# Optimization experiments

Hardware: AMD Instinct MI355X
Metric: run time of the kernel (lower is better)

## Reference

```python
import jax, jax.numpy as jnp
import numpy as np
import math

NUM_HEADS = 12
BLOCK_N = 32  # key-block size used by the Triton kernel for head_dim <= 64


def _apply_rope(x, cos, sin):
    # x: [B,H,S,D]; cos/sin: [S, D//2] -> interleaved-pair RoPE (matches apply_rope_rse)
    c = cos[None, None, :, :]
    s = sin[None, None, :, :]
    xe = x[..., 0::2]
    xo = x[..., 1::2]
    re = xe * c - xo * s
    ro = xo * c + xe * s
    return jnp.stack([re, ro], axis=-1).reshape(x.shape)


def setup_inputs() -> dict:
    key = jax.random.key(0)
    ks = jax.random.split(key, 9)
    B, S, HID = 16, 1024, 768
    D = HID // NUM_HEADS
    x = jax.random.normal(ks[0], (B, S, HID), jnp.float32)
    init = lambda k: jax.random.normal(k, (HID, HID), jnp.float32) * 0.02
    Wq, Wk, Wv, Wo = init(ks[1]), init(ks[2]), init(ks[3]), init(ks[4])
    bq = jnp.zeros((HID,), jnp.float32)
    bk = jnp.zeros((HID,), jnp.float32)
    bv = jnp.zeros((HID,), jnp.float32)
    bo = jnp.zeros((HID,), jnp.float32)
    lam = jnp.array(0.01, jnp.float32)
    # RoPE caches [S, D//2]
    inv_freq = 1.0 / (10000.0 ** (jnp.arange(0, D, 2, dtype=jnp.float32) / D))
    ang = jnp.arange(S, dtype=jnp.float32)[:, None] * inv_freq[None, :]
    cos_cache = jnp.cos(ang)
    sin_cache = jnp.sin(ang)
    return {"x": x, "Wq": Wq, "bq": bq, "Wk": Wk, "bk": bk, "Wv": Wv, "bv": bv,
            "Wo": Wo, "bo": bo, "lam": lam, "cos_cache": cos_cache, "sin_cache": sin_cache}


def _rse_attention(q, k, v, cos_cache, sin_cache, lam):
    # q,k,v: [B,H,S,D]. Block-sequential stick-breaking with online stats,
    # faithfully reproducing the Triton kernel's math (causal=False).
    B, H, S, D = q.shape
    scale = 1.0 / math.sqrt(D)
    qs = _apply_rope(q, cos_cache, sin_cache) * scale
    kr = _apply_rope(k, cos_cache, sin_cache)
    nb = S // BLOCK_N
    kb = jnp.moveaxis(kr.reshape(B, H, nb, BLOCK_N, D), 2, 0)  # [nb,B,H,BN,D]
    vb = jnp.moveaxis(v.reshape(B, H, nb, BLOCK_N, D), 2, 0)   # [nb,B,H,BN,D]
    pos_m = jnp.arange(S, dtype=jnp.float32)
    pb = jnp.arange(S, dtype=jnp.float32).reshape(nb, BLOCK_N)

    def step(carry, inp):
        rem, acc, l_i, m_i = carry
        kblk, vblk, pblk = inp
        decay = lam * jnp.abs(pos_m[:, None] - pblk[None, :])  # [S,BN]
        logits = jnp.einsum('bhmd,bhnd->bhmn', qs, kblk) - decay[None, None]
        beta = jax.nn.sigmoid(jnp.clip(logits, -20.0, 20.0))
        w = beta * rem[..., None]                 # [B,H,S,BN]
        consumed = jnp.sum(w, axis=-1)            # [B,H,S]
        rem_new = jnp.maximum(rem * (1.0 - consumed), 1e-6)
        acc_new = acc + jnp.einsum('bhmn,bhnd->bhmd', w, vblk)
        m_new = jnp.maximum(m_i, jnp.max(logits, axis=-1))
        alpha = jnp.exp2(m_i - m_new)
        l_new = l_i * alpha + consumed
        return (rem_new, acc_new, l_new, m_new), None

    rem0 = jnp.ones((B, H, S), jnp.float32)
    acc0 = jnp.zeros((B, H, S, D), jnp.float32)
    l0 = jnp.zeros((B, H, S), jnp.float32)
    m0 = jnp.full((B, H, S), -jnp.inf, jnp.float32)
    (rem, acc, l_i, m_i), _ = jax.lax.scan(step, (rem0, acc0, l0, m0), (kb, vb, pb))
    return acc / jnp.maximum(l_i, 1e-6)[..., None]


def reference(x, Wq, bq, Wk, bk, Wv, bv, Wo, bo, lam, cos_cache, sin_cache):
    B, S, HID = x.shape
    H = NUM_HEADS
    D = HID // H
    to_heads = lambda t: t.reshape(B, S, H, D).transpose(0, 2, 1, 3)
    q = to_heads(x @ Wq.T + bq)
    k = to_heads(x @ Wk.T + bk)
    v = to_heads(x @ Wv.T + bv)
    o = _rse_attention(q, k, v, cos_cache, sin_cache, lam)  # [B,H,S,D]
    ctx = o.transpose(0, 2, 1, 3).reshape(B, S, HID)
    return ctx @ Wo.T + bo
```

## Files before the change

kernel.cpp:

```cpp
#include <hip/hip_runtime.h>
#include <math.h>

#define NH    12
#define SEQ   1024
#define DH    64
#define HID   768
#define BATCH 16
#define MTOT  (BATCH*SEQ)
#define KDIM  HID

typedef __attribute__((ext_vector_type(8))) short short8;
typedef __attribute__((ext_vector_type(4))) short short4v;
typedef __attribute__((ext_vector_type(8))) unsigned short ushort8;
typedef __attribute__((ext_vector_type(4))) float float4v;

__device__ __forceinline__ float bf2f(unsigned short u) {
    union { unsigned int i; float f; } v; v.i = ((unsigned int)u) << 16; return v.f;
}
__device__ __forceinline__ unsigned short f2bf(float f) {
    union { float f; unsigned int i; } v; v.f = f;
    unsigned int x = v.i;
    return (unsigned short)((x + 0x7FFFu + ((x >> 16) & 1u)) >> 16);
}
__device__ __forceinline__ float loadf(const void* p, size_t i, bool f32) {
    return f32 ? ((const float*)p)[i] : bf2f(((const unsigned short*)p)[i]);
}
__device__ __forceinline__ unsigned int cvt_pk_bf16(float a, float b) {
    unsigned int r;
    asm("v_cvt_pk_bf16_f32 %0, %1, %2" : "=v"(r) : "v"(a), "v"(b));
    return r;
}
__device__ __forceinline__ float fast_exp2(float x) {
#if __has_builtin(__builtin_amdgcn_exp2f)
    return __builtin_amdgcn_exp2f(x);
#else
    return exp2f(x);
#endif
}

__device__ __forceinline__ void gload_lds16(const void* g, void* l) {
    __builtin_amdgcn_global_load_lds(
        (const __attribute__((address_space(1))) unsigned int*)g,
        (__attribute__((address_space(3))) unsigned int*)l, 16, 0, 0);
}

__global__ __launch_bounds__(256) void detect_kernel(
    const unsigned short* __restrict__ x, unsigned int* __restrict__ flag)
{
    __shared__ int cnt[256];
    const int tid = threadIdx.x;
    int local = 0;
    for (int i = tid; i < 1024; i += 256) {
        const unsigned short u = x[i];
        const int e = (u >> 7) & 0xFF;
        if ((e >= 96 && e <= 134) || ((u & 0x7FFF) == 0)) local++;
    }
    cnt[tid] = local;
    __syncthreads();
    for (int s = 128; s > 0; s >>= 1) {
        if (tid < s) cnt[tid] += cnt[tid + s];
        __syncthreads();
    }
    if (tid == 0) flag[0] = (cnt[0] < 900) ? 1u : 0u;
}

template<bool LO>
__global__ __launch_bounds__(256) void split_ker(
    const void* __restrict__ src, const unsigned int* __restrict__ flag,
    unsigned short* __restrict__ hi, unsigned short* __restrict__ lo, int n)
{
    const size_t i = ((size_t)blockIdx.x * 256 + threadIdx.x) * 8;
    if (i >= (size_t)n) return;
    ushort8 h, l;
    if (flag[0]) {
        const float* fp = (const float*)src + i;
        float4v f0 = *(const float4v*)fp, f1 = *(const float4v*)(fp + 4);
#pragma unroll
        for (int e = 0; e < 4; e++) {
            unsigned short h0 = f2bf(f0[e]), h1 = f2bf(f1[e]);
            h[e] = h0; h[4 + e] = h1;
            if (LO) { l[e] = f2bf(f0[e] - bf2f(h0)); l[4 + e] = f2bf(f1[e] - bf2f(h1)); }
        }
    } else {
        h = *(const ushort8*)((const unsigned short*)src + i);
        if (LO) {
#pragma unroll
            for (int e = 0; e < 8; e++) l[e] = 0;
        }
    }
    *(ushort8*)(hi + i) = h;
    if (LO) *(ushort8*)(lo + i) = l;
}

template<bool WF32, bool PRECISE>
__device__ __forceinline__ void loadW(const void* __restrict__ W, size_t idx,
                                      short8& hi, short8& lo) {
    if constexpr (WF32) {
        const float* fp = (const float*)W + idx;
        float4v f0 = *(const float4v*)fp, f1 = *(const float4v*)(fp + 4);
#pragma unroll
        for (int e = 0; e < 4; e++) {
            unsigned short h0 = f2bf(f0[e]), h1 = f2bf(f1[e]);
            hi[e] = (short)h0; hi[4 + e] = (short)h1;
            if constexpr (PRECISE) {
                lo[e] = (short)f2bf(f0[e] - bf2f(h0));
                lo[4 + e] = (short)f2bf(f1[e] - bf2f(h1));
            }
        }
    } else {
        hi = *(const short8*)((const unsigned short*)W + idx);
        if constexpr (PRECISE) {
#pragma unroll
            for (int e = 0; e < 8; e++) lo[e] = 0;
        }
    }
}

template<bool PRECISE, bool WPRE, bool WF32>
__device__ __forceinline__ void staged_kloop(
    const unsigned short* __restrict__ Ahi, const unsigned short* __restrict__ Alo,
    const void* __restrict__ Wa, const void* __restrict__ Wb,
    unsigned short* sAhi, unsigned short* sAlo,
    int m_blk0, int n_base, int wid, int lane, float4v acc[4][4])
{
    const int tid  = wid * 64 + lane;
    const int quad = lane >> 4, l16 = lane & 15;
    const int m_off = (wid >> 1) * 64;
    const int srow = tid >> 2;
    const int scc  = tid & 3;

    auto stage = [&](int k0, int b) {
#pragma unroll
        for (int it = 0; it < 2; it++) {
            const int r = it * 64 + srow;
            const size_t gidx = (size_t)(m_blk0 + r) * KDIM + k0 + scc * 8;
            const int loff = b * 4096 + r * 32 + scc * 8;
            gload_lds16(Ahi + gidx, sAhi + loff);
            if constexpr (PRECISE) gload_lds16(Alo + gidx, sAlo + loff);
        }
    };

    stage(0, 0);
    __syncthreads();

    for (int k0 = 0; k0 < KDIM; k0 += 32) {
        const int b = (k0 >> 5) & 1;
        if (k0 + 32 < KDIM) stage(k0 + 32, b ^ 1);

        short8 bh[4], bl[4];
#pragma unroll
        for (int in = 0; in < 4; in++) {
            const size_t widx = (size_t)(n_base + in * 16 + l16) * KDIM + k0 + quad * 8;
            if constexpr (WPRE) {
                bh[in] = *(const short8*)((const unsigned short*)Wa + widx);
                if constexpr (PRECISE)
                    bl[in] = *(const short8*)((const unsigned short*)Wb + widx);
            } else {
                loadW<WF32, PRECISE>(Wa, widx, bh[in], bl[in]);
            }
        }
        short8 ah[4], al[4];
#pragma unroll
        for (int im = 0; im < 4; im++) {
            const int r = m_off + im * 16 + l16;
            ah[im] = *(const short8*)(sAhi + b * 4096 + r * 32 + quad * 8);
            if constexpr (PRECISE) al[im] = *(const short8*)(sAlo + b * 4096 + r * 32 + quad * 8);
        }
#pragma unroll
        for (int im = 0; im < 4; im++)
#pragma unroll
            for (int in = 0; in < 4; in++) {
                acc[im][in] = __builtin_amdgcn_mfma_f32_16x16x32_bf16(
                    ah[im], bh[in], acc[im][in], 0, 0, 0);
                if constexpr (PRECISE) {
                    acc[im][in] = __builtin_amdgcn_mfma_f32_16x16x32_bf16(
                        al[im], bh[in], acc[im][in], 0, 0, 0);
                    acc[im][in] = __builtin_amdgcn_mfma_f32_16x16x32_bf16(
                        ah[im], bl[in], acc[im][in], 0, 0, 0);
                }
            }
        __syncthreads();
    }
}

template<int MODE, bool WPRE>
__device__ __forceinline__ void gemm_body(
    const unsigned short* __restrict__ Ahi, const unsigned short* __restrict__ Alo,
    const void* __restrict__ Wa, const void* __restrict__ Wb,
    const void* __restrict__ bias,
    const void* __restrict__ cosc, const void* __restrict__ sinc,
    const unsigned int* __restrict__ flag,
    void* __restrict__ Out, void* __restrict__ Out2,
    unsigned short* sAhi, unsigned short* sAlo,
    int m_blk0, int ny)
{
    constexpr bool PRECISE = (MODE <= 1);
    const int tid  = threadIdx.x;
    const int wid  = tid >> 6;
    const int lane = tid & 63;
    const int quad = lane >> 4;
    const int l16  = lane & 15;
    const int m_blk = m_blk0 + (wid >> 1) * 64;
    const int n_base = ny * 128 + (wid & 1) * 64;
    const bool f32 = (flag[0] != 0u);

    float4v acc[4][4];
#pragma unroll
    for (int i = 0; i < 4; i++)
#pragma unroll
        for (int j = 0; j < 4; j++) acc[i][j] = (float4v)(0.f);

    if constexpr (WPRE) {
        staged_kloop<PRECISE, true, false>(Ahi, Alo, Wa, Wb, sAhi, sAlo,
                                           m_blk0, n_base, wid, lane, acc);
    } else {
        if (f32) staged_kloop<PRECISE, false, true >(Ahi, Alo, Wa, Wb, sAhi, sAlo,
                                                     m_blk0, n_base, wid, lane, acc);
        else     staged_kloop<PRECISE, false, false>(Ahi, Alo, Wa, Wb, sAhi, sAlo,
                                                     m_blk0, n_base, wid, lane, acc);
    }

#pragma unroll
    for (int im = 0; im < 4; im++) {
#pragma unroll
        for (int in = 0; in < 4; in++) {
            const int col = n_base + in * 16 + l16;
            const float bval = loadf(bias, col, f32);
            if constexpr (MODE == 2) {
                short4v pk;
#pragma unroll
                for (int r = 0; r < 4; r++)
                    pk[r] = (short)f2bf(acc[im][in][r] + bval);
                const int row = m_blk + im * 16 + quad * 4;
                const int b = row >> 10, s = row & (SEQ - 1);
                const int h = col >> 6, d = col & (DH - 1);
                *(short4v*)((unsigned short*)Out +
                    ((size_t)(b * NH + h) * DH + d) * SEQ + s) = pk;
            } else if constexpr (MODE <= 1) {
                const int d  = col & (DH - 1);
                const int d2 = d >> 1;
#pragma unroll
                for (int r = 0; r < 4; r++) {
                    const int row = m_blk + im * 16 + quad * 4 + r;
                    const int s  = row & (SEQ - 1);
                    const float v = acc[im][in][r] + bval;
                    const float c  = loadf(cosc, s * (DH / 2) + d2, f32);
                    const float sn = loadf(sinc, s * (DH / 2) + d2, f32);
                    const float p = __shfl_xor(v, 1);
                    float o = (d & 1) ? (v * c + p * sn) : (v * c - p * sn);
                    if (MODE == 0) o *= 0.18033688f;
                    const float po = __shfl_xor(o, 1);
                    if (!(l16 & 1)) {
                        const unsigned short h0 = f2bf(o), h1 = f2bf(po);
                        const unsigned short l0 = f2bf(o - bf2f(h0));
                        const unsigned short l1 = f2bf(po - bf2f(h1));
                        const int b = row >> 10, h = col >> 6;
                        const size_t idx = ((size_t)(b * NH + h) * SEQ + s) * DH + d;
                        *(unsigned int*)((unsigned short*)Out + idx) =
                            (unsigned int)h0 | ((unsigned int)h1 << 16);
                        *(unsigned int*)((unsigned short*)Out2 + idx) =
                            (unsigned int)l0 | ((unsigned int)l1 << 16);
                    }
                }
            } else {
#pragma unroll
                for (int r = 0; r < 4; r++) {
                    const int row = m_blk + im * 16 + quad * 4 + r;
                    const float v = acc[im][in][r] + bval;
                    if (f32) ((float*)Out)[(size_t)row * HID + col] = v;
                    else     ((unsigned short*)Out)[(size_t)row * HID + col] = f2bf(v);
                }
            }
        }
    }
}

template<int MODE, bool WPRE>
__global__ __launch_bounds__(256) void gemm_staged(
    const unsigned short* __restrict__ Ahi, const unsigned short* __restrict__ Alo,
    const void* __restrict__ Wa, const void* __restrict__ Wb,
    const void* __restrict__ bias,
    const void* __restrict__ cosc, const void* __restrict__ sinc,
    const unsigned int* __restrict__ flag,
    void* __restrict__ Out, void* __restrict__ Out2)
{
    constexpr bool PRECISE = (MODE <= 1);
    __shared__ unsigned short sAhi[2 * 4096];
    __shared__ unsigned short sAlo[PRECISE ? 2 * 4096 : 64];
    gemm_body<MODE, WPRE>(Ahi, Alo, Wa, Wb, bias, cosc, sinc, flag, Out, Out2,
                          sAhi, sAlo, blockIdx.x * 128, blockIdx.y);
}

template<bool WPRE>
__global__ __launch_bounds__(256) void gemm_qkv(
    const unsigned short* __restrict__ Ahi, const unsigned short* __restrict__ Alo,
    const void* __restrict__ Wqa, const void* __restrict__ Wqb,
    const void* __restrict__ Wka, const void* __restrict__ Wkb,
    const void* __restrict__ Wva,
    const void* __restrict__ bq, const void* __restrict__ bk,
    const void* __restrict__ bv,
    const void* __restrict__ cosc, const void* __restrict__ sinc,
    const unsigned int* __restrict__ flag,
    void* __restrict__ Qhi, void* __restrict__ Qlo,
    void* __restrict__ Khi, void* __restrict__ Klo,
    void* __restrict__ Vt)
{
    __shared__ unsigned short sAhi[2 * 4096];
    __shared__ unsigned short sAlo[2 * 4096];
    const int which = blockIdx.y / 6;
    const int ny    = blockIdx.y % 6;
    const int m0    = blockIdx.x * 128;
    if (which == 0)
        gemm_body<0, WPRE>(Ahi, Alo, Wqa, Wqb, bq, cosc, sinc, flag,
                           Qhi, Qlo, sAhi, sAlo, m0, ny);
    else if (which == 1)
        gemm_body<1, WPRE>(Ahi, Alo, Wka, Wkb, bk, cosc, sinc, flag,
                           Khi, Klo, sAhi, sAlo, m0, ny);
    else
        gemm_body<2, WPRE>(Ahi, nullptr, Wva, nullptr, bv, nullptr, nullptr, flag,
                           Vt, nullptr, sAhi, sAlo, m0, ny);
}

__global__ __launch_bounds__(256, 2) void attn_mfma(
    const unsigned short* __restrict__ Qhi, const unsigned short* __restrict__ Qlo,
    const unsigned short* __restrict__ Khi, const unsigned short* __restrict__ Klo,
    const unsigned short* __restrict__ Vt,
    const void* __restrict__ lam_p, const unsigned int* __restrict__ flag,
    unsigned short* __restrict__ ctx)
{
    const int tid  = threadIdx.x;
    const int wid  = tid >> 6;
    const int lane = tid & 63;
    const int quad = lane >> 4;
    const int l16  = lane & 15;
    const int phys = blockIdx.x;
    const int virt = (phys & 7) * 96 + (phys >> 3);
    const int bh   = virt >> 2;
    const int q0   = (virt & 3) * 256 + wid * 64;
    const bool f32 = (flag[0] != 0u);
    const float lam2 = loadf(lam_p, 0, f32) * 1.44269504f;

    __shared__ unsigned short KV[2][6144];

    const int krow = tid >> 3, kch = tid & 7;
    const int kgch = kch ^ (krow & 7);
    const int vrow = tid >> 2, vch = tid & 3;
    const int vgch = vch ^ (vrow & 3);

    #define STAGE(kb_, buf_) do {                                            \
        const size_t gk = ((size_t)bh * SEQ + (kb_) * 32 + krow) * DH + kgch * 8; \
        gload_lds16(Khi + gk, &KV[buf_][0]    + tid * 8);                    \
        gload_lds16(Klo + gk, &KV[buf_][2048] + tid * 8);                    \
        const size_t gv = ((size_t)bh * DH + vrow) * SEQ + (kb_) * 32 + vgch * 8; \
        gload_lds16(Vt + gv, &KV[buf_][4096] + tid * 8);                     \
    } while (0)

    short8 qh[4][2], ql[4][2];
#pragma unroll
    for (int qn = 0; qn < 4; qn++)
#pragma unroll
        for (int ks = 0; ks < 2; ks++) {
            const size_t base = ((size_t)bh * SEQ + (q0 + qn * 16 + l16)) * DH
                                + ks * 32 + quad * 8;
            qh[qn][ks] = *(const short8*)(Qhi + base);
            ql[qn][ks] = *(const short8*)(Qlo + base);
        }

    float4v acc_o[4][4];
#pragma unroll
    for (int i = 0; i < 4; i++)
#pragma unroll
        for (int j = 0; j < 4; j++) acc_o[i][j] = (float4v)(0.f);

    float rem[4] = {1.f, 1.f, 1.f, 1.f};
    float l_i[4] = {0.f, 0.f, 0.f, 0.f};
    float m_i[4] = {-INFINITY, -INFINITY, -INFINITY, -INFINITY};
    float qf[4];
#pragma unroll
    for (int qn = 0; qn < 4; qn++) qf[qn] = (float)(q0 + qn * 16 + l16);

    STAGE(0, 0);
    __syncthreads();

    for (int kb = 0; kb < SEQ / 32; kb++) {
        const int buf = kb & 1;
        if (kb + 1 < SEQ / 32) STAGE(kb + 1, buf ^ 1);

        short8 kh[2][2], kl[2][2];
#pragma unroll
        for (int kt = 0; kt < 2; kt++)
#pragma unroll
            for (int ks = 0; ks < 2; ks++) {
                const int off = (kt * 16 + l16) * 64
                                + ((ks * 4 + quad) ^ (l16 & 7)) * 8;
                kh[kt][ks] = *(const short8*)(&KV[buf][0]    + off);
                kl[kt][ks] = *(const short8*)(&KV[buf][2048] + off);
            }

        float4v s[2][4];
#pragma unroll
        for (int kt = 0; kt < 2; kt++)
#pragma unroll
            for (int qn = 0; qn < 4; qn++) s[kt][qn] = (float4v)(0.f);
#pragma unroll
        for (int ks = 0; ks < 2; ks++)
#pragma unroll
            for (int kt = 0; kt < 2; kt++)
#pragma unroll
                for (int qn = 0; qn < 4; qn++) {
                    s[kt][qn] = __builtin_amdgcn_mfma_f32_16x16x32_bf16(
                        kh[kt][ks], qh[qn][ks], s[kt][qn], 0, 0, 0);
                    s[kt][qn] = __builtin_amdgcn_mfma_f32_16x16x32_bf16(
                        kl[kt][ks], qh[qn][ks], s[kt][qn], 0, 0, 0);
                    s[kt][qn] = __builtin_amdgcn_mfma_f32_16x16x32_bf16(
                        kh[kt][ks], ql[qn][ks], s[kt][qn], 0, 0, 0);
                }

        float cons[4] = {0.f, 0.f, 0.f, 0.f};
        float mx[4] = {-INFINITY, -INFINITY, -INFINITY, -INFINITY};
#pragma unroll
        for (int kt = 0; kt < 2; kt++)
#pragma unroll
            for (int qn = 0; qn < 4; qn++)
#pragma unroll
                for (int r = 0; r < 4; r++) {
                    const float keyf = (float)(kb * 32 + kt * 16 + quad * 4 + r);
                    const float logit = s[kt][qn][r] - lam2 * fabsf(qf[qn] - keyf);
                    mx[qn] = fmaxf(mx[qn], logit);
                    const float beta = __builtin_amdgcn_rcpf(
                        1.f + fast_exp2(-logit));
                    const float w = beta * rem[qn];
                    cons[qn] += w;
                    s[kt][qn][r] = w;
                }
#pragma unroll
        for (int qn = 0; qn < 4; qn++) {
            cons[qn] += __shfl_xor(cons[qn], 16);
            cons[qn] += __shfl_xor(cons[qn], 32);
            mx[qn] = fmaxf(mx[qn], __shfl_xor(mx[qn], 16));
            mx[qn] = fmaxf(mx[qn], __shfl_xor(mx[qn], 32));
        }

        short8 pf[4];
#pragma unroll
        for (int qn = 0; qn < 4; qn++) {
            const unsigned int d00 = cvt_pk_bf16(s[0][qn][0], s[0][qn][1]);
            const unsigned int d01 = cvt_pk_bf16(s[0][qn][2], s[0][qn][3]);
            const unsigned int d10 = cvt_pk_bf16(s[1][qn][0], s[1][qn][1]);
            const unsigned int d11 = cvt_pk_bf16(s[1][qn][2], s[1][qn][3]);
            auto r0 = __builtin_amdgcn_permlane32_swap(d00, d10, false, false);
            auto r1 = __builtin_amdgcn_permlane32_swap(d01, d11, false, false);
            auto t0 = __builtin_amdgcn_permlane16_swap(r0[0], r0[1], false, false);
            auto t1 = __builtin_amdgcn_permlane16_swap(r1[0], r1[1], false, false);
            union { unsigned int u[4]; short8 s8; } cv;
            cv.u[0] = t0[0];
            cv.u[1] = t1[0];
            cv.u[2] = t0[1];
            cv.u[3] = t1[1];
            pf[qn] = cv.s8;
        }

        short8 vf[4];
#pragma unroll
        for (int dt = 0; dt < 4; dt++) {
            const int off = (dt * 16 + l16) * 32 + (quad ^ (l16 & 3)) * 8;
            vf[dt] = *(const short8*)(&KV[buf][4096] + off);
        }
#pragma unroll
        for (int dt = 0; dt < 4; dt++)
#pragma unroll
            for (int jn = 0; jn < 4; jn++)
                acc_o[dt][jn] = __builtin_amdgcn_mfma_f32_16x16x32_bf16(
                    vf[dt], pf[jn], acc_o[dt][jn], 0, 0, 0);

#pragma unroll
        for (int qn = 0; qn < 4; qn++) {
            rem[qn] = fmaxf(rem[qn] * (1.f - cons[qn]), 1e-6f);
            const float m_new = fmaxf(m_i[qn], mx[qn]);
            const float alpha = fast_exp2((m_i[qn] - m_new) * 0.69314718f);
            l_i[qn] = l_i[qn] * alpha + cons[qn];
            m_i[qn] = m_new;
        }

        __syncthreads();
    }

    const int b = bh / NH, h = bh % NH;
    float inv[4];
#pragma unroll
    for (int jn = 0; jn < 4; jn++)
        inv[jn] = __builtin_amdgcn_rcpf(fmaxf(l_i[jn], 1e-6f));
#pragma unroll
    for (int dt = 0; dt < 4; dt++)
#pragma unroll
        for (int jn = 0; jn < 4; jn++) {
            short4v pk;
#pragma unroll
            for (int r = 0; r < 4; r++)
                pk[r] = (short)f2bf(acc_o[dt][jn][r] * inv[jn]);
            const int q_g = q0 + jn * 16 + l16;
            *(short4v*)(ctx + ((size_t)(b * SEQ + q_g) * HID
                               + h * DH + dt * 16 + quad * 4)) = pk;
        }
    #undef STAGE
}

extern "C" void kernel_launch(void* const* d_in, const int* in_sizes, int n_in,
                              void* d_out, int out_size, void* d_ws, size_t ws_size,
                              hipStream_t stream) {
    const void* x    = d_in[0];
    const void* Wq   = d_in[1];
    const void* bq   = d_in[2];
    const void* Wk   = d_in[3];
    const void* bk   = d_in[4];
    const void* Wv   = d_in[5];
    const void* bv   = d_in[6];
    const void* Wo   = d_in[7];
    const void* bo   = d_in[8];
    const void* lam  = d_in[9];
    const void* cosc = d_in[10];
    const void* sinc = d_in[11];

    const size_t NELEM = (size_t)MTOT * HID;
    const size_t WELEM = (size_t)HID * HID;
    unsigned int* flag = (unsigned int*)d_ws;
    unsigned short* Xhi = (unsigned short*)((char*)d_ws + 64);
    unsigned short* Xlo = Xhi + NELEM;
    unsigned short* Qhi = Xlo + NELEM;
    unsigned short* Qlo = Qhi + NELEM;
    unsigned short* Wqh = Qlo + NELEM;
    unsigned short* Wql = Wqh + WELEM;
    unsigned short* Wkh = Wql + WELEM;
    unsigned short* Wkl = Wkh + WELEM;
    unsigned short* Wvh = Wkl + WELEM;
    unsigned short* Woh = Wvh + WELEM;
    unsigned short* VtF = Woh + WELEM;
    const size_t NEED  = 64 + 4 * NELEM * 2 + 6 * WELEM * 2;
    const size_t NEEDF = NEED + NELEM * 2;
    const bool wpre = (ws_size >= NEED);
    const bool fuse = (ws_size >= NEEDF);

    unsigned short* Vt  = fuse ? VtF : Xlo;
    unsigned short* Ctx = Xhi;
    unsigned short* Khi = (unsigned short*)d_out;
    unsigned short* Klo = Khi + NELEM;

    detect_kernel<<<1, 256, 0, stream>>>((const unsigned short*)x, flag);
    split_ker<true><<<(MTOT * KDIM) / 2048, 256, 0, stream>>>(x, flag, Xhi, Xlo, MTOT * KDIM);

    dim3 gg(MTOT / 128, HID / 128), gb(256);
    if (fuse) {
        const int wb = (int)(WELEM / 2048);
        split_ker<true ><<<wb, 256, 0, stream>>>(Wq, flag, Wqh, Wql, (int)WELEM);
        split_ker<true ><<<wb, 256, 0, stream>>>(Wk, flag, Wkh, Wkl, (int)WELEM);
        split_ker<false><<<wb, 256, 0, stream>>>(Wv, flag, Wvh, nullptr, (int)WELEM);
        split_ker<false><<<wb, 256, 0, stream>>>(Wo, flag, Woh, nullptr, (int)WELEM);
        gemm_qkv<true><<<dim3(MTOT / 128, 18), gb, 0, stream>>>(
            Xhi, Xlo, Wqh, Wql, Wkh, Wkl, Wvh, bq, bk, bv,
            cosc, sinc, flag, Qhi, Qlo, Khi, Klo, VtF);
    } else if (wpre) {
        const int wb = (int)(WELEM / 2048);
        split_ker<true ><<<wb, 256, 0, stream>>>(Wq, flag, Wqh, Wql, (int)WELEM);
        split_ker<true ><<<wb, 256, 0, stream>>>(Wk, flag, Wkh, Wkl, (int)WELEM);
        split_ker<false><<<wb, 256, 0, stream>>>(Wv, flag, Wvh, nullptr, (int)WELEM);
        split_ker<false><<<wb, 256, 0, stream>>>(Wo, flag, Woh, nullptr, (int)WELEM);
        gemm_staged<0, true><<<gg, gb, 0, stream>>>(Xhi, Xlo, Wqh, Wql, bq, cosc, sinc, flag, Qhi, Qlo);
        gemm_staged<1, true><<<gg, gb, 0, stream>>>(Xhi, Xlo, Wkh, Wkl, bk, cosc, sinc, flag, Khi, Klo);
        gemm_staged<2, true><<<gg, gb, 0, stream>>>(Xhi, nullptr, Wvh, nullptr, bv, nullptr, nullptr, flag, Vt, nullptr);
    } else {
        gemm_staged<0, false><<<gg, gb, 0, stream>>>(Xhi, Xlo, Wq, nullptr, bq, cosc, sinc, flag, Qhi, Qlo);
        gemm_staged<1, false><<<gg, gb, 0, stream>>>(Xhi, Xlo, Wk, nullptr, bk, cosc, sinc, flag, Khi, Klo);
        gemm_staged<2, false><<<gg, gb, 0, stream>>>(Xhi, nullptr, Wv, nullptr, bv, nullptr, nullptr, flag, Vt, nullptr);
    }
    attn_mfma<<<dim3(4 * BATCH * NH), 256, 0, stream>>>(
        Qhi, Qlo, Khi, Klo, Vt, lam, flag, Ctx);
    if (wpre)
        gemm_staged<3, true><<<gg, gb, 0, stream>>>(Ctx, nullptr, Woh, nullptr, bo, nullptr, nullptr, flag, d_out, nullptr);
    else
        gemm_staged<3, false><<<gg, gb, 0, stream>>>(Ctx, nullptr, Wo, nullptr, bo, nullptr, nullptr, flag, d_out, nullptr);
}
```

Before: 665.9 us.

## Load GEMM A operands directly from global and interleave independent MFMA chains

Replaces the LDS double-buffered staging of the A operand in the projection GEMMs with direct per-wave global loads of the MFMA fragments. This removes the shared memory allocation and the per-iteration block barrier. In exchange, reuse of A across the two column-half waves now comes from cache instead of LDS. It also reorders the MFMA sequences in both the GEMM and the attention score computation, so that consecutive instructions target different accumulators rather than chaining on the same one, which is meant to hide MFMA dependency latency.

```diff
diff --git a/kernel.cpp b/kernel.cpp
--- a/kernel.cpp
+++ b/kernel.cpp
@@ -117,40 +117,32 @@
 }
 
 template<bool PRECISE, bool WPRE, bool WF32>
-__device__ __forceinline__ void staged_kloop(
+__device__ __forceinline__ void direct_kloop(
     const unsigned short* __restrict__ Ahi, const unsigned short* __restrict__ Alo,
     const void* __restrict__ Wa, const void* __restrict__ Wb,
-    unsigned short* sAhi, unsigned short* sAlo,
-    int m_blk0, int n_base, int wid, int lane, float4v acc[4][4])
-{
-    const int tid  = wid * 64 + lane;
+    int m_blk, int n_base, int lane, float4v acc[4][4])
+{
     const int quad = lane >> 4, l16 = lane & 15;
-    const int m_off = (wid >> 1) * 64;
-    const int srow = tid >> 2;
-    const int scc  = tid & 3;
-
-    auto stage = [&](int k0, int b) {
-#pragma unroll
-        for (int it = 0; it < 2; it++) {
-            const int r = it * 64 + srow;
-            const size_t gidx = (size_t)(m_blk0 + r) * KDIM + k0 + scc * 8;
-            const int loff = b * 4096 + r * 32 + scc * 8;
-            gload_lds16(Ahi + gidx, sAhi + loff);
-            if constexpr (PRECISE) gload_lds16(Alo + gidx, sAlo + loff);
-        }
-    };
-
-    stage(0, 0);
-    __syncthreads();
-
-    for (int k0 = 0; k0 < KDIM; k0 += 32) {
-        const int b = (k0 >> 5) & 1;
-        if (k0 + 32 < KDIM) stage(k0 + 32, b ^ 1);
-
+    constexpr int NT = KDIM / 32;
+
+    const unsigned short* A0h = Ahi + (size_t)(m_blk + l16) * KDIM;
+    const unsigned short* A0l = Alo ? Alo + (size_t)(m_blk + l16) * KDIM : nullptr;
+
+#pragma unroll 2
+    for (int kt = 0; kt < NT; kt++) {
+        const int kc = kt * 32 + quad * 8;
+
+        short8 ah[4], al[4];
+#pragma unroll
+        for (int im = 0; im < 4; im++) {
+            ah[im] = *(const short8*)(A0h + (size_t)(im * 16) * KDIM + kc);
+            if constexpr (PRECISE)
+                al[im] = *(const short8*)(A0l + (size_t)(im * 16) * KDIM + kc);
+        }
         short8 bh[4], bl[4];
 #pragma unroll
         for (int in = 0; in < 4; in++) {
-            const size_t widx = (size_t)(n_base + in * 16 + l16) * KDIM + k0 + quad * 8;
+            const size_t widx = (size_t)(n_base + in * 16 + l16) * KDIM + kc;
             if constexpr (WPRE) {
                 bh[in] = *(const short8*)((const unsigned short*)Wa + widx);
                 if constexpr (PRECISE)
@@ -159,27 +151,26 @@
                 loadW<WF32, PRECISE>(Wa, widx, bh[in], bl[in]);
             }
         }
-        short8 ah[4], al[4];
-#pragma unroll
-        for (int im = 0; im < 4; im++) {
-            const int r = m_off + im * 16 + l16;
-            ah[im] = *(const short8*)(sAhi + b * 4096 + r * 32 + quad * 8);
-            if constexpr (PRECISE) al[im] = *(const short8*)(sAlo + b * 4096 + r * 32 + quad * 8);
-        }
 #pragma unroll
         for (int im = 0; im < 4; im++)
 #pragma unroll
-            for (int in = 0; in < 4; in++) {
+            for (int in = 0; in < 4; in++)
                 acc[im][in] = __builtin_amdgcn_mfma_f32_16x16x32_bf16(
                     ah[im], bh[in], acc[im][in], 0, 0, 0);
-                if constexpr (PRECISE) {
+        if constexpr (PRECISE) {
+#pragma unroll
+            for (int im = 0; im < 4; im++)
+#pragma unroll
+                for (int in = 0; in < 4; in++)
                     acc[im][in] = __builtin_amdgcn_mfma_f32_16x16x32_bf16(
                         al[im], bh[in], acc[im][in], 0, 0, 0);
+#pragma unroll
+            for (int im = 0; im < 4; im++)
+#pragma unroll
+                for (int in = 0; in < 4; in++)
                     acc[im][in] = __builtin_amdgcn_mfma_f32_16x16x32_bf16(
                         ah[im], bl[in], acc[im][in], 0, 0, 0);
-                }
-            }
-        __syncthreads();
+        }
     }
 }
 
@@ -191,7 +182,6 @@
     const void* __restrict__ cosc, const void* __restrict__ sinc,
     const unsigned int* __restrict__ flag,
     void* __restrict__ Out, void* __restrict__ Out2,
-    unsigned short* sAhi, unsigned short* sAlo,
     int m_blk0, int ny)
 {
     constexpr bool PRECISE = (MODE <= 1);
@@ -211,13 +201,13 @@
         for (int j = 0; j < 4; j++) acc[i][j] = (float4v)(0.f);
 
     if constexpr (WPRE) {
-        staged_kloop<PRECISE, true, false>(Ahi, Alo, Wa, Wb, sAhi, sAlo,
-                                           m_blk0, n_base, wid, lane, acc);
+        direct_kloop<PRECISE, true, false>(Ahi, Alo, Wa, Wb,
+                                           m_blk, n_base, lane, acc);
     } else {
-        if (f32) staged_kloop<PRECISE, false, true >(Ahi, Alo, Wa, Wb, sAhi, sAlo,
-                                                     m_blk0, n_base, wid, lane, acc);
-        else     staged_kloop<PRECISE, false, false>(Ahi, Alo, Wa, Wb, sAhi, sAlo,
-                                                     m_blk0, n_base, wid, lane, acc);
+        if (f32) direct_kloop<PRECISE, false, true >(Ahi, Alo, Wa, Wb,
+                                                     m_blk, n_base, lane, acc);
+        else     direct_kloop<PRECISE, false, false>(Ahi, Alo, Wa, Wb,
+                                                     m_blk, n_base, lane, acc);
     }
 
 #pragma unroll
@@ -284,11 +274,8 @@
     const unsigned int* __restrict__ flag,
     void* __restrict__ Out, void* __restrict__ Out2)
 {
-    constexpr bool PRECISE = (MODE <= 1);
-    __shared__ unsigned short sAhi[2 * 4096];
-    __shared__ unsigned short sAlo[PRECISE ? 2 * 4096 : 64];
     gemm_body<MODE, WPRE>(Ahi, Alo, Wa, Wb, bias, cosc, sinc, flag, Out, Out2,
-                          sAhi, sAlo, blockIdx.x * 128, blockIdx.y);
+                          blockIdx.x * 128, blockIdx.y);
 }
 
 template<bool WPRE>
@@ -305,20 +292,18 @@
     void* __restrict__ Khi, void* __restrict__ Klo,
     void* __restrict__ Vt)
 {
-    __shared__ unsigned short sAhi[2 * 4096];
-    __shared__ unsigned short sAlo[2 * 4096];
     const int which = blockIdx.y / 6;
     const int ny    = blockIdx.y % 6;
     const int m0    = blockIdx.x * 128;
     if (which == 0)
         gemm_body<0, WPRE>(Ahi, Alo, Wqa, Wqb, bq, cosc, sinc, flag,
-                           Qhi, Qlo, sAhi, sAlo, m0, ny);
+                           Qhi, Qlo, m0, ny);
     else if (which == 1)
         gemm_body<1, WPRE>(Ahi, Alo, Wka, Wkb, bk, cosc, sinc, flag,
-                           Khi, Klo, sAhi, sAlo, m0, ny);
+                           Khi, Klo, m0, ny);
     else
         gemm_body<2, WPRE>(Ahi, nullptr, Wva, nullptr, bv, nullptr, nullptr, flag,
-                           Vt, nullptr, sAhi, sAlo, m0, ny);
+                           Vt, nullptr, m0, ny);
 }
 
 __global__ __launch_bounds__(256, 2) void attn_mfma(
@@ -403,18 +388,26 @@
 #pragma unroll
             for (int qn = 0; qn < 4; qn++) s[kt][qn] = (float4v)(0.f);
 #pragma unroll
-        for (int ks = 0; ks < 2; ks++)
+        for (int ks = 0; ks < 2; ks++) {
 #pragma unroll
             for (int kt = 0; kt < 2; kt++)
 #pragma unroll
-                for (int qn = 0; qn < 4; qn++) {
+                for (int qn = 0; qn < 4; qn++)
                     s[kt][qn] = __builtin_amdgcn_mfma_f32_16x16x32_bf16(
                         kh[kt][ks], qh[qn][ks], s[kt][qn], 0, 0, 0);
+#pragma unroll
+            for (int kt = 0; kt < 2; kt++)
+#pragma unroll
+                for (int qn = 0; qn < 4; qn++)
                     s[kt][qn] = __builtin_amdgcn_mfma_f32_16x16x32_bf16(
                         kl[kt][ks], qh[qn][ks], s[kt][qn], 0, 0, 0);
+#pragma unroll
+            for (int kt = 0; kt < 2; kt++)
+#pragma unroll
+                for (int qn = 0; qn < 4; qn++)
                     s[kt][qn] = __builtin_amdgcn_mfma_f32_16x16x32_bf16(
                         kh[kt][ks], ql[qn][ks], s[kt][qn], 0, 0, 0);
-                }
+        }
 
         float cons[4] = {0.f, 0.f, 0.f, 0.f};
         float mx[4] = {-INFINITY, -INFINITY, -INFINITY, -INFINITY};
```

New measurement: 702.2 us. 1.05x slower.
